# Performance work log

Hardware: AMD Instinct MI355X
Metric: run time of the kernel (lower is better)

## Reference

```python
import jax, jax.numpy as jnp
import numpy as np

B, L, S, DE, D = 16, 2048, 1024, 512, 256
VOP, NSIL, A, NN = 64, 8, 64, 100000


def setup_inputs() -> dict:
    key = jax.random.key(0)
    ks = jax.random.split(key, 11)
    return {
        "encoded_sentence_tokens": jax.random.normal(ks[0], (B, S, DE), jnp.float32),
        "encoded_stack_nodes": jax.random.normal(ks[1], (NN, D), jnp.float32),
        "silent_embeddings": jax.random.normal(ks[2], (NSIL, D), jnp.float32),
        "op_embedding": jax.random.normal(ks[3], (VOP, D), jnp.float32) * 0.02,
        "w_shift": jax.random.normal(ks[4], (DE, D), jnp.float32) / np.sqrt(DE).astype(np.float32),
        "b_shift": jnp.zeros((D,), jnp.float32),
        "op_tokens": jax.random.randint(ks[5], (B, L), 0, VOP),
        "arg_idx": jax.random.randint(ks[6], (B, L), 0, NSIL + A),
        "shift_idx": jax.random.randint(ks[7], (B, L), 0, S),
        "item_type": jax.random.randint(ks[8], (B, L), 0, 3),
        "avail_nodes": jax.random.randint(ks[9], (B, L, A), 0, NN),
    }


def reference(encoded_sentence_tokens, encoded_stack_nodes, silent_embeddings,
              op_embedding, w_shift, b_shift,
              op_tokens, arg_idx, shift_idx, item_type, avail_nodes):
    # Operation embeddings: [B, L, D]
    emb_ops = op_embedding[op_tokens]

    # Shift-arg embeddings: gather sentence encodings per (b, l), then linear. [B, L, D]
    gathered_sent = jnp.take_along_axis(
        encoded_sentence_tokens, shift_idx[:, :, None], axis=1)  # [B, L, DE]
    emb_shift = jnp.einsum('ble,ed->bld', gathered_sent, w_shift) + b_shift

    # Argument embeddings: choice index < NSIL -> silent embedding, else stack node.
    # Equivalent to concat([silent, available_node_embs], axis=2)[arg_idx] without
    # materializing the [B, L, NSIL+A, D] choice tensor.
    is_silent = arg_idx < NSIL                                    # [B, L]
    silent_sel = silent_embeddings[jnp.clip(arg_idx, 0, NSIL - 1)]  # [B, L, D]
    node_pos = jnp.clip(arg_idx - NSIL, 0, A - 1)                 # [B, L]
    node_ids = jnp.take_along_axis(avail_nodes, node_pos[:, :, None], axis=2)[..., 0]
    node_sel = encoded_stack_nodes[node_ids]                      # [B, L, D]
    emb_args = jnp.where(is_silent[:, :, None], silent_sel, node_sel)

    # combine_embeddings: positional masks align, so it's a 3-way select by type.
    t = item_type[:, :, None]
    result = jnp.where(t == 0, emb_ops,
             jnp.where(t == 1, emb_args,
             jnp.where(t == 2, emb_shift, jnp.zeros_like(emb_ops))))
    return result
```

## Files before the change

### kernel.cpp

```cpp
#include <hip/hip_runtime.h>

#define B_    16
#define L_    2048
#define S_    1024
#define DE_   512
#define D_    256
#define NSIL_ 8
#define A_    64
#define MS_   (B_ * S_)

#define BM 128
#define BN 64
#define BK 64
#define NGEMM 512
#define NT01  256

typedef __attribute__((ext_vector_type(8))) short  short8;
typedef __attribute__((ext_vector_type(4))) float  f32x4;

__device__ __forceinline__ unsigned short f2bf(float f) {
    unsigned int x = __builtin_bit_cast(unsigned int, f);
    x += 0x7fffu + ((x >> 16) & 1u);
    return (unsigned short)(x >> 16);
}
__device__ __forceinline__ float bf2f(unsigned short u) {
    unsigned int x = ((unsigned int)u) << 16;
    return __builtin_bit_cast(float, x);
}

__global__ __launch_bounds__(256) void srse_wt(
    const float* __restrict__ w, unsigned short* __restrict__ wT)
{
    const int k = blockIdx.x;
    const int n = threadIdx.x;
    wT[n * DE_ + k] = f2bf(w[k * D_ + n]);
}

__global__ __launch_bounds__(256) void srse_gemm_t01(
    const float*          __restrict__ sent,
    const unsigned short* __restrict__ wT,
    const float*          __restrict__ bsh,
    unsigned short*       __restrict__ Pb,
    const float*          __restrict__ op_emb,
    const float*          __restrict__ silent,
    const float*          __restrict__ nodes,
    const int*            __restrict__ op_tokens,
    const int*            __restrict__ arg_idx,
    const int*            __restrict__ item_type,
    const int*            __restrict__ avail,
    float*                __restrict__ out)
{
    __shared__ alignas(16) unsigned short As[BM * BK];
    __shared__ alignas(16) unsigned short Bs[BN * BK];

    const int t    = threadIdx.x;
    const int lane = t & 63;
    const int wid  = t >> 6;

    if (blockIdx.x < NGEMM) {
        const int wg  = (blockIdx.x & 7) * (NGEMM / 8) + (blockIdx.x >> 3);
        const int bm  = wg >> 2;
        const int bn  = wg & 3;
        const int gm0 = bm * BM;
        const int gn0 = bn * BN;

        const int wm = wid & 1;
        const int wn = wid >> 1;
        const int fr = lane & 15;
        const int fq = lane >> 4;

        f32x4 acc[4][2] = {};

        for (int k0 = 0; k0 < DE_; k0 += BK) {
            #pragma unroll
            for (int s = 0; s < 4; ++s) {
                const int id  = s * 256 + t;
                const int row = id >> 3;
                const int k8  = id & 7;
                const float4 a0 = *(const float4*)(sent + (size_t)(gm0 + row) * DE_ + k0 + k8 * 8);
                const float4 a1 = *(const float4*)(sent + (size_t)(gm0 + row) * DE_ + k0 + k8 * 8 + 4);
                short8 v;
                v[0] = f2bf(a0.x); v[1] = f2bf(a0.y); v[2] = f2bf(a0.z); v[3] = f2bf(a0.w);
                v[4] = f2bf(a1.x); v[5] = f2bf(a1.y); v[6] = f2bf(a1.z); v[7] = f2bf(a1.w);
                const int widx = (row * BK + k8 * 8) ^ ((row & 7) << 3);
                *(short8*)(As + widx) = v;
            }
            #pragma unroll
            for (int s = 0; s < 2; ++s) {
                const int id = s * 256 + t;
                const int n  = id >> 3;
                const int k8 = id & 7;
                short8 v = *(const short8*)(wT + (size_t)(gn0 + n) * DE_ + k0 + k8 * 8);
                const int widx = (n * BK + k8 * 8) ^ ((n & 7) << 3);
                *(short8*)(Bs + widx) = v;
            }
            __syncthreads();

            #pragma unroll
            for (int ks = 0; ks < 2; ++ks) {
                short8 af[4], bfr[2];
                #pragma unroll
                for (int mf = 0; mf < 4; ++mf) {
                    const int row = wm * 64 + mf * 16 + fr;
                    af[mf] = *(const short8*)(As + ((row * BK + ks * 32 + fq * 8) ^ ((row & 7) << 3)));
                }
                #pragma unroll
                for (int nf = 0; nf < 2; ++nf) {
                    const int n = wn * 32 + nf * 16 + fr;
                    bfr[nf] = *(const short8*)(Bs + ((n * BK + ks * 32 + fq * 8) ^ ((n & 7) << 3)));
                }
                #pragma unroll
                for (int mf = 0; mf < 4; ++mf)
                    #pragma unroll
                    for (int nf = 0; nf < 2; ++nf)
                        acc[mf][nf] = __builtin_amdgcn_mfma_f32_16x16x32_bf16(
                            af[mf], bfr[nf], acc[mf][nf], 0, 0, 0);
            }
            __syncthreads();
        }

        #pragma unroll
        for (int nf = 0; nf < 2; ++nf) {
            const int col = gn0 + wn * 32 + nf * 16 + fr;
            const float bval = bsh[col];
            #pragma unroll
            for (int mf = 0; mf < 4; ++mf) {
                #pragma unroll
                for (int r = 0; r < 4; ++r) {
                    const int row = gm0 + wm * 64 + mf * 16 + fq * 4 + r;
                    Pb[(size_t)row * D_ + col] = f2bf(acc[mf][nf][r] + bval);
                }
            }
        }
    } else {
        const int bid2 = blockIdx.x - NGEMM;
        const int r0w  = bid2 * 128 + wid * 32;

        #pragma unroll
        for (int b4 = 0; b4 < 4; ++b4) {
            const int r0 = r0w + b4 * 8;
            const float* src[8];
            int tt8[8];
            #pragma unroll
            for (int i = 0; i < 8; ++i) {
                const int row = r0 + i;
                const int tt  = item_type[row];
                tt8[i] = tt;
                const int a = arg_idx[row];
                int np = a - NSIL_;
                np = np < 0 ? 0 : (np > A_ - 1 ? A_ - 1 : np);
                const float* s0 = op_emb + (size_t)op_tokens[row] * D_;
                const float* s1 = (a < NSIL_)
                                  ? silent + (size_t)a * D_
                                  : nodes + (size_t)avail[(size_t)row * A_ + np] * D_;
                src[i] = (tt == 0) ? s0 : s1;
            }
            float4 v[8];
            #pragma unroll
            for (int i = 0; i < 8; ++i)
                v[i] = *(const float4*)(src[i] + lane * 4);
            #pragma unroll
            for (int i = 0; i < 8; ++i)
                if (tt8[i] != 2)
                    *(float4*)(out + (size_t)(r0 + i) * D_ + lane * 4) = v[i];
        }
    }
}

__global__ __launch_bounds__(256) void srse_t2(
    const unsigned short* __restrict__ Pb,
    const int*            __restrict__ shift_idx,
    const int*            __restrict__ item_type,
    float*                __restrict__ out)
{
    const int wid  = threadIdx.x >> 6;
    const int lane = threadIdx.x & 63;
    const int r0   = blockIdx.x * 64 + wid * 16;

    int tt[16], ss[16];
    #pragma unroll
    for (int i = 0; i < 16; ++i) tt[i] = item_type[r0 + i];
    #pragma unroll
    for (int i = 0; i < 16; ++i) ss[i] = shift_idx[r0 + i];

    #pragma unroll
    for (int i = 0; i < 16; ++i) {
        if (tt[i] == 2) {
            const int row = r0 + i;
            const int b   = row >> 11;
            const unsigned short* p = Pb + (size_t)((b << 10) + ss[i]) * D_;
            const short4 x = *(const short4*)(p + lane * 4);
            float4 o;
            o.x = bf2f((unsigned short)x.x);
            o.y = bf2f((unsigned short)x.y);
            o.z = bf2f((unsigned short)x.z);
            o.w = bf2f((unsigned short)x.w);
            *(float4*)(out + (size_t)row * D_ + lane * 4) = o;
        }
    }
}

extern "C" void kernel_launch(void* const* d_in, const int* in_sizes, int n_in,
                              void* d_out, int out_size, void* d_ws, size_t ws_size,
                              hipStream_t stream) {
    const float* sent      = (const float*)d_in[0];
    const float* nodes     = (const float*)d_in[1];
    const float* silent    = (const float*)d_in[2];
    const float* op_emb    = (const float*)d_in[3];
    const float* w         = (const float*)d_in[4];
    const float* bsh       = (const float*)d_in[5];
    const int*   op_tokens = (const int*)d_in[6];
    const int*   arg_idx   = (const int*)d_in[7];
    const int*   shift_idx = (const int*)d_in[8];
    const int*   item_type = (const int*)d_in[9];
    const int*   avail     = (const int*)d_in[10];
    float*       out       = (float*)d_out;

    unsigned short* wT = (unsigned short*)d_ws;
    unsigned short* Pb = (unsigned short*)((char*)d_ws + D_ * DE_ * 2);

    srse_wt<<<DE_, 256, 0, stream>>>(w, wT);

    srse_gemm_t01<<<NGEMM + NT01, 256, 0, stream>>>(
        sent, wT, bsh, Pb, op_emb, silent, nodes,
        op_tokens, arg_idx, item_type, avail, out);

    srse_t2<<<(B_ * L_) / 64, 256, 0, stream>>>(Pb, shift_idx, item_type, out);
}
```

Before: 217.8 us.

## Retile GEMM to full-width N tiles and fuse weight conversion into it

Changes the GEMM tile from 128x64 to 64x256 with 512-thread blocks, so each block covers the full output width. Each row of the fp32 sentence matrix is now read and converted once instead of once per N tile. The separate transpose/bf16 kernel for the weights is removed: each block loads fp32 w directly, converts it and packs pairs into the swizzled LDS layout. This saves a launch and workspace traffic, but every block now redoes the weight conversion and issues many scalar 32-bit LDS stores. The gather part is reindexed so 8 waves cover 256 rows per block.

Result: slower. 223.9 us (+2.8%).

```diff
diff --git a/kernel.cpp b/kernel.cpp
--- a/kernel.cpp
+++ b/kernel.cpp
@@ -9,11 +9,11 @@
 #define A_    64
 #define MS_   (B_ * S_)
 
-#define BM 128
-#define BN 64
+#define BM 64
+#define BN 256
 #define BK 64
-#define NGEMM 512
-#define NT01  256
+#define NGEMM (MS_ / BM)
+#define NT01  128
 
 typedef __attribute__((ext_vector_type(8))) short  short8;
 typedef __attribute__((ext_vector_type(4))) float  f32x4;
@@ -28,17 +28,9 @@
     return __builtin_bit_cast(float, x);
 }
 
-__global__ __launch_bounds__(256) void srse_wt(
-    const float* __restrict__ w, unsigned short* __restrict__ wT)
-{
-    const int k = blockIdx.x;
-    const int n = threadIdx.x;
-    wT[n * DE_ + k] = f2bf(w[k * D_ + n]);
-}
-
-__global__ __launch_bounds__(256) void srse_gemm_t01(
+__global__ __launch_bounds__(512) void srse_gemm_t01(
     const float*          __restrict__ sent,
-    const unsigned short* __restrict__ wT,
+    const float*          __restrict__ w,
     const float*          __restrict__ bsh,
     unsigned short*       __restrict__ Pb,
     const float*          __restrict__ op_emb,
@@ -58,61 +50,60 @@
     const int wid  = t >> 6;
 
     if (blockIdx.x < NGEMM) {
-        const int wg  = (blockIdx.x & 7) * (NGEMM / 8) + (blockIdx.x >> 3);
-        const int bm  = wg >> 2;
-        const int bn  = wg & 3;
-        const int gm0 = bm * BM;
-        const int gn0 = bn * BN;
-
-        const int wm = wid & 1;
-        const int wn = wid >> 1;
-        const int fr = lane & 15;
-        const int fq = lane >> 4;
-
-        f32x4 acc[4][2] = {};
+        const int gm0 = blockIdx.x * BM;
+        const int wm  = wid & 1;
+        const int wn  = wid >> 1;
+        const int fr  = lane & 15;
+        const int fq  = lane >> 4;
+
+        f32x4 acc[2][4] = {};
 
         for (int k0 = 0; k0 < DE_; k0 += BK) {
-            #pragma unroll
-            for (int s = 0; s < 4; ++s) {
-                const int id  = s * 256 + t;
-                const int row = id >> 3;
-                const int k8  = id & 7;
+            {
+                const int row = t >> 3;
+                const int k8  = t & 7;
                 const float4 a0 = *(const float4*)(sent + (size_t)(gm0 + row) * DE_ + k0 + k8 * 8);
                 const float4 a1 = *(const float4*)(sent + (size_t)(gm0 + row) * DE_ + k0 + k8 * 8 + 4);
                 short8 v;
                 v[0] = f2bf(a0.x); v[1] = f2bf(a0.y); v[2] = f2bf(a0.z); v[3] = f2bf(a0.w);
                 v[4] = f2bf(a1.x); v[5] = f2bf(a1.y); v[6] = f2bf(a1.z); v[7] = f2bf(a1.w);
-                const int widx = (row * BK + k8 * 8) ^ ((row & 7) << 3);
-                *(short8*)(As + widx) = v;
-            }
-            #pragma unroll
-            for (int s = 0; s < 2; ++s) {
-                const int id = s * 256 + t;
-                const int n  = id >> 3;
-                const int k8 = id & 7;
-                short8 v = *(const short8*)(wT + (size_t)(gn0 + n) * DE_ + k0 + k8 * 8);
-                const int widx = (n * BK + k8 * 8) ^ ((n & 7) << 3);
-                *(short8*)(Bs + widx) = v;
+                *(short8*)(As + ((row * BK + k8 * 8) ^ ((row & 7) << 3))) = v;
+            }
+            #pragma unroll
+            for (int p = 0; p < 4; ++p) {
+                const int kk = p * 16 + (t >> 6) * 2;
+                const int n4 = t & 63;
+                const float4 b0 = *(const float4*)(w + (size_t)(k0 + kk)     * D_ + n4 * 4);
+                const float4 b1 = *(const float4*)(w + (size_t)(k0 + kk + 1) * D_ + n4 * 4);
+                const float b0a[4] = {b0.x, b0.y, b0.z, b0.w};
+                const float b1a[4] = {b1.x, b1.y, b1.z, b1.w};
+                #pragma unroll
+                for (int i = 0; i < 4; ++i) {
+                    const int n = n4 * 4 + i;
+                    const unsigned int v = (unsigned int)f2bf(b0a[i])
+                                         | ((unsigned int)f2bf(b1a[i]) << 16);
+                    *(unsigned int*)(Bs + ((n * BK + kk) ^ ((n & 7) << 3))) = v;
+                }
             }
             __syncthreads();
 
             #pragma unroll
             for (int ks = 0; ks < 2; ++ks) {
-                short8 af[4], bfr[2];
-                #pragma unroll
-                for (int mf = 0; mf < 4; ++mf) {
-                    const int row = wm * 64 + mf * 16 + fr;
+                short8 af[2], bfr[4];
+                #pragma unroll
+                for (int mf = 0; mf < 2; ++mf) {
+                    const int row = wm * 32 + mf * 16 + fr;
                     af[mf] = *(const short8*)(As + ((row * BK + ks * 32 + fq * 8) ^ ((row & 7) << 3)));
                 }
                 #pragma unroll
-                for (int nf = 0; nf < 2; ++nf) {
-                    const int n = wn * 32 + nf * 16 + fr;
+                for (int nf = 0; nf < 4; ++nf) {
+                    const int n = wn * 64 + nf * 16 + fr;
                     bfr[nf] = *(const short8*)(Bs + ((n * BK + ks * 32 + fq * 8) ^ ((n & 7) << 3)));
                 }
                 #pragma unroll
-                for (int mf = 0; mf < 4; ++mf)
+                for (int mf = 0; mf < 2; ++mf)
                     #pragma unroll
-                    for (int nf = 0; nf < 2; ++nf)
+                    for (int nf = 0; nf < 4; ++nf)
                         acc[mf][nf] = __builtin_amdgcn_mfma_f32_16x16x32_bf16(
                             af[mf], bfr[nf], acc[mf][nf], 0, 0, 0);
             }
@@ -120,21 +111,21 @@
         }
 
         #pragma unroll
-        for (int nf = 0; nf < 2; ++nf) {
-            const int col = gn0 + wn * 32 + nf * 16 + fr;
+        for (int nf = 0; nf < 4; ++nf) {
+            const int col = wn * 64 + nf * 16 + fr;
             const float bval = bsh[col];
             #pragma unroll
-            for (int mf = 0; mf < 4; ++mf) {
+            for (int mf = 0; mf < 2; ++mf) {
                 #pragma unroll
                 for (int r = 0; r < 4; ++r) {
-                    const int row = gm0 + wm * 64 + mf * 16 + fq * 4 + r;
+                    const int row = gm0 + wm * 32 + mf * 16 + fq * 4 + r;
                     Pb[(size_t)row * D_ + col] = f2bf(acc[mf][nf][r] + bval);
                 }
             }
         }
     } else {
         const int bid2 = blockIdx.x - NGEMM;
-        const int r0w  = bid2 * 128 + wid * 32;
+        const int r0w  = bid2 * 256 + wid * 32;
 
         #pragma unroll
         for (int b4 = 0; b4 < 4; ++b4) {
@@ -216,13 +207,10 @@
     const int*   avail     = (const int*)d_in[10];
     float*       out       = (float*)d_out;
 
-    unsigned short* wT = (unsigned short*)d_ws;
-    unsigned short* Pb = (unsigned short*)((char*)d_ws + D_ * DE_ * 2);
-
-    srse_wt<<<DE_, 256, 0, stream>>>(w, wT);
-
-    srse_gemm_t01<<<NGEMM + NT01, 256, 0, stream>>>(
-        sent, wT, bsh, Pb, op_emb, silent, nodes,
+    unsigned short* Pb = (unsigned short*)d_ws;
+
+    srse_gemm_t01<<<NGEMM + NT01, 512, 0, stream>>>(
+        sent, w, bsh, Pb, op_emb, silent, nodes,
         op_tokens, arg_idx, item_type, avail, out);
 
     srse_t2<<<(B_ * L_) / 64, 256, 0, stream>>>(Pb, shift_idx, item_type, out);
```
